# Kernel optimization log

Hardware: AMD Instinct MI355X
Metric: run time of the kernel (lower is better)

The kernel has to match this reference:

```python
import jax, jax.numpy as jnp
from jax import lax
import numpy as np

K = 8  # box-filter / unfold kernel size


def setup_inputs() -> dict:
    key = jax.random.key(0)
    k1, k2 = jax.random.split(key)
    a, b, h, w = 8, 64, 256, 256
    x = jax.random.normal(k1, (a, b, h, w), dtype=jnp.float32)
    local_count = jax.random.uniform(k2, (a, 1, h - K + 1, w - K + 1), dtype=jnp.float32)
    return {"x": x, "local_count": local_count, "output_stride": 8}


def reference(x, local_count, output_stride):
    # output_stride is accepted but unused, matching the original module.
    a, b, h, w = x.shape
    Hp, Wp = h - K + 1, w - K + 1
    L = Hp * Wp

    avg = jnp.mean(x, axis=1, keepdims=True)          # (a,1,h,w)
    sm = jnp.exp(avg)
    # 8x8 all-ones conv2d (valid) == box sum over 8x8 windows
    sc = lax.reduce_window(sm, jnp.float32(0), lax.add,
                           (1, 1, K, K), (1, 1, 1, 1), 'VALID')  # (a,1,Hp,Wp)

    # F.unfold(sm, kernel_size=8): (a, 64, L); C=1 so patch ordering is row-major (i*K+j)
    patches = lax.conv_general_dilated_patches(sm, (K, K), (1, 1), 'VALID')  # (a,64,Hp,Wp)
    uf = patches.reshape(a, K * K, L)

    ssc = sc.reshape(a, 1, L)                # broadcast over 64 patch rows (== torch.tile)
    c = local_count.reshape(a, 1, L)
    R = uf / ssc * c                         # (a,64,L)

    # F.fold(R, (h,w), kernel_size=8): overlap-add of 8x8 patches
    Rg = R.reshape(a, K, K, Hp, Wp)
    out = jnp.zeros((a, 1, h, w), dtype=x.dtype)
    for i in range(K):
        for j in range(K):
            out = out.at[:, 0, i:i + Hp, j:j + Wp].add(Rg[:, i, j])
    return out
```

## Files before the change

### kernel.cpp

```cpp
#include <hip/hip_runtime.h>

#define KK 8
#define NA 8
#define NB 64
#define NH 256
#define NW 256
#define HP (NH - KK + 1)
#define WP (NW - KK + 1)

__global__ __launch_bounds__(256) void k_mean_exp(const float* __restrict__ x,
                                                 float* __restrict__ sm) {
    int tid = blockIdx.x * blockDim.x + threadIdx.x;
    int a = tid >> 14;
    int p4 = (tid & 16383);
    const float4* xp = (const float4*)(x + (size_t)a * NB * NH * NW) + p4;
    const int cs = NH * NW / 4;
    float4 acc = {0.f, 0.f, 0.f, 0.f};
    #pragma unroll 8
    for (int b = 0; b < NB; ++b) {
        float4 v = xp[(size_t)b * cs];
        acc.x += v.x; acc.y += v.y; acc.z += v.z; acc.w += v.w;
    }
    const float s = 1.0f / NB;
    float4 r;
    r.x = __expf(acc.x * s);
    r.y = __expf(acc.y * s);
    r.z = __expf(acc.z * s);
    r.w = __expf(acc.w * s);
    ((float4*)sm)[tid] = r;
}

__global__ __launch_bounds__(256) void k_sc_t(const float* __restrict__ sm,
                                              const float* __restrict__ c,
                                              float* __restrict__ t) {
    int tid = blockIdx.x * blockDim.x + threadIdx.x;
    if (tid >= NA * HP * WP) return;
    int a = tid / (HP * WP);
    int rem = tid - a * (HP * WP);
    int ph = rem / WP;
    int pw = rem - ph * WP;
    const float* s = sm + ((size_t)a * NH + ph) * NW + pw;
    float sum = 0.f;
    #pragma unroll
    for (int i = 0; i < KK; ++i) {
        #pragma unroll
        for (int j = 0; j < KK; ++j) sum += s[i * NW + j];
    }
    t[tid] = c[tid] / sum;
}

__global__ __launch_bounds__(256) void k_out(const float* __restrict__ sm,
                                             const float* __restrict__ t,
                                             float* __restrict__ out) {
    int tid = blockIdx.x * blockDim.x + threadIdx.x;
    int a = tid >> 16;
    int rem = tid & 65535;
    int y = rem >> 8;
    int x = rem & 255;
    int ph0 = y - (KK - 1); if (ph0 < 0) ph0 = 0;
    int ph1 = y; if (ph1 > HP - 1) ph1 = HP - 1;
    int pw0 = x - (KK - 1); if (pw0 < 0) pw0 = 0;
    int pw1 = x; if (pw1 > WP - 1) pw1 = WP - 1;
    const float* tp = t + (size_t)a * HP * WP;
    float sum = 0.f;
    for (int ph = ph0; ph <= ph1; ++ph) {
        const float* row = tp + ph * WP;
        for (int pw = pw0; pw <= pw1; ++pw) sum += row[pw];
    }
    out[tid] = sm[tid] * sum;
}

extern "C" void kernel_launch(void* const* d_in, const int* in_sizes, int n_in,
                              void* d_out, int out_size, void* d_ws, size_t ws_size,
                              hipStream_t stream) {
    const float* x = (const float*)d_in[0];
    const float* c = (const float*)d_in[1];
    float* out = (float*)d_out;
    float* sm = (float*)d_ws;
    float* t  = sm + (size_t)NA * NH * NW;

    k_mean_exp<<<(NA * NH * NW / 4) / 256, 256, 0, stream>>>(x, sm);
    k_sc_t<<<(NA * HP * WP + 255) / 256, 256, 0, stream>>>(sm, c, t);
    k_out<<<(NA * NH * NW) / 256, 256, 0, stream>>>(sm, t, out);
}
```

Before: 216.1 us.

## Split channel reduction four ways and fuse box-sum and fold stages in shared memory

```diff
diff --git a/kernel.cpp b/kernel.cpp
--- a/kernel.cpp
+++ b/kernel.cpp
@@ -7,67 +7,83 @@
 #define NW 256
 #define HP (NH - KK + 1)
 #define WP (NW - KK + 1)
+#define QSTRIDE (NA * NH * NW)
 
-__global__ __launch_bounds__(256) void k_mean_exp(const float* __restrict__ x,
-                                                 float* __restrict__ sm) {
-    int tid = blockIdx.x * blockDim.x + threadIdx.x;
-    int a = tid >> 14;
-    int p4 = (tid & 16383);
-    const float4* xp = (const float4*)(x + (size_t)a * NB * NH * NW) + p4;
-    const int cs = NH * NW / 4;
+__global__ __launch_bounds__(256) void k_partial(const float* __restrict__ x,
+                                                 float* __restrict__ ps) {
+    int tid = blockIdx.x * 256 + threadIdx.x;
+    int q   = tid >> 17;
+    int rem = tid & 131071;
+    int a   = rem >> 14;
+    int p4  = rem & 16383;
+    const float4* xp = (const float4*)(x + ((size_t)a * NB + q * 16) * (NH * NW)) + p4;
     float4 acc = {0.f, 0.f, 0.f, 0.f};
-    #pragma unroll 8
-    for (int b = 0; b < NB; ++b) {
-        float4 v = xp[(size_t)b * cs];
+    #pragma unroll
+    for (int b = 0; b < 16; ++b) {
+        float4 v = xp[(size_t)b * (NH * NW / 4)];
         acc.x += v.x; acc.y += v.y; acc.z += v.z; acc.w += v.w;
     }
-    const float s = 1.0f / NB;
-    float4 r;
-    r.x = __expf(acc.x * s);
-    r.y = __expf(acc.y * s);
-    r.z = __expf(acc.z * s);
-    r.w = __expf(acc.w * s);
-    ((float4*)sm)[tid] = r;
+    ((float4*)ps)[tid] = acc;
 }
 
-__global__ __launch_bounds__(256) void k_sc_t(const float* __restrict__ sm,
-                                              const float* __restrict__ c,
-                                              float* __restrict__ t) {
-    int tid = blockIdx.x * blockDim.x + threadIdx.x;
-    if (tid >= NA * HP * WP) return;
-    int a = tid / (HP * WP);
-    int rem = tid - a * (HP * WP);
-    int ph = rem / WP;
-    int pw = rem - ph * WP;
-    const float* s = sm + ((size_t)a * NH + ph) * NW + pw;
-    float sum = 0.f;
+__global__ __launch_bounds__(1024) void k_fused(const float* __restrict__ ps,
+                                                const float* __restrict__ cnt,
+                                                float* __restrict__ out) {
+    __shared__ float s_sm[46 * 48];
+    __shared__ float hrs[46 * 40];
+    __shared__ float t_s[39 * 40];
+    __shared__ float vs[32 * 40];
+    const int tx = threadIdx.x, ty = threadIdx.y;
+    const int tid = ty * 32 + tx;
+    const int a = blockIdx.z;
+    const int y0 = blockIdx.y * 32, x0 = blockIdx.x * 32;
+    const float* pa = ps + (size_t)a * (NH * NW);
+
+    for (int idx = tid; idx < 46 * 46; idx += 1024) {
+        int r = idx / 46, cc = idx - r * 46;
+        int rg = y0 - 7 + r;  rg = rg < 0 ? 0 : (rg > NH - 1 ? NH - 1 : rg);
+        int cg = x0 - 7 + cc; cg = cg < 0 ? 0 : (cg > NW - 1 ? NW - 1 : cg);
+        int p = rg * NW + cg;
+        float s = pa[p] + pa[p + QSTRIDE] + pa[p + 2 * QSTRIDE] + pa[p + 3 * QSTRIDE];
+        s_sm[r * 48 + cc] = __expf(s * (1.0f / NB));
+    }
+    __syncthreads();
+
+    for (int idx = tid; idx < 46 * 39; idx += 1024) {
+        int r = idx / 39, cc = idx - r * 39;
+        const float* row = &s_sm[r * 48 + cc];
+        hrs[r * 40 + cc] = row[0] + row[1] + row[2] + row[3] +
+                           row[4] + row[5] + row[6] + row[7];
+    }
+    __syncthreads();
+
+    const float* ca = cnt + (size_t)a * (HP * WP);
+    for (int idx = tid; idx < 39 * 39; idx += 1024) {
+        int r = idx / 39, cc = idx - r * 39;
+        float sc = 0.f;
+        #pragma unroll
+        for (int i = 0; i < 8; ++i) sc += hrs[(r + i) * 40 + cc];
+        int ph = y0 - 7 + r, pw = x0 - 7 + cc;
+        float tv = 0.f;
+        if ((unsigned)ph < (unsigned)HP && (unsigned)pw < (unsigned)WP)
+            tv = ca[ph * WP + pw] / sc;
+        t_s[r * 40 + cc] = tv;
+    }
+    __syncthreads();
+
+    for (int idx = tid; idx < 32 * 39; idx += 1024) {
+        int r = idx / 39, cc = idx - r * 39;
+        float s = 0.f;
+        #pragma unroll
+        for (int i = 0; i < 8; ++i) s += t_s[(r + i) * 40 + cc];
+        vs[r * 40 + cc] = s;
+    }
+    __syncthreads();
+
+    float s = 0.f;
     #pragma unroll
-    for (int i = 0; i < KK; ++i) {
-        #pragma unroll
-        for (int j = 0; j < KK; ++j) sum += s[i * NW + j];
-    }
-    t[tid] = c[tid] / sum;
-}
-
-__global__ __launch_bounds__(256) void k_out(const float* __restrict__ sm,
-                                             const float* __restrict__ t,
-                                             float* __restrict__ out) {
-    int tid = blockIdx.x * blockDim.x + threadIdx.x;
-    int a = tid >> 16;
-    int rem = tid & 65535;
-    int y = rem >> 8;
-    int x = rem & 255;
-    int ph0 = y - (KK - 1); if (ph0 < 0) ph0 = 0;
-    int ph1 = y; if (ph1 > HP - 1) ph1 = HP - 1;
-    int pw0 = x - (KK - 1); if (pw0 < 0) pw0 = 0;
-    int pw1 = x; if (pw1 > WP - 1) pw1 = WP - 1;
-    const float* tp = t + (size_t)a * HP * WP;
-    float sum = 0.f;
-    for (int ph = ph0; ph <= ph1; ++ph) {
-        const float* row = tp + ph * WP;
-        for (int pw = pw0; pw <= pw1; ++pw) sum += row[pw];
-    }
-    out[tid] = sm[tid] * sum;
+    for (int j = 0; j < 8; ++j) s += vs[ty * 40 + tx + j];
+    out[((size_t)a * NH + (y0 + ty)) * NW + (x0 + tx)] = s_sm[(ty + 7) * 48 + tx + 7] * s;
 }
 
 extern "C" void kernel_launch(void* const* d_in, const int* in_sizes, int n_in,
@@ -76,10 +92,10 @@
     const float* x = (const float*)d_in[0];
     const float* c = (const float*)d_in[1];
     float* out = (float*)d_out;
-    float* sm = (float*)d_ws;
-    float* t  = sm + (size_t)NA * NH * NW;
+    float* ps  = (float*)d_ws;
 
-    k_mean_exp<<<(NA * NH * NW / 4) / 256, 256, 0, stream>>>(x, sm);
-    k_sc_t<<<(NA * HP * WP + 255) / 256, 256, 0, stream>>>(sm, c, t);
-    k_out<<<(NA * NH * NW) / 256, 256, 0, stream>>>(sm, t, out);
+    k_partial<<<2048, 256, 0, stream>>>(x, ps);
+    dim3 grid(NW / 32, NH / 32, NA);
+    dim3 block(32, 32);
+    k_fused<<<grid, block, 0, stream>>>(ps, c, out);
 }
```

Result: faster. 201.3 us (-6.9%).
